# Optimization experiments

Measured on AMD Instinct MI355X. Metric: run time of the kernel, lower is better.

Reference implementation:

```python
import jax, jax.numpy as jnp
import numpy as np

B, T, D, H, L = 256, 128, 512, 512, 3  # batch, T, input_size, hidden_size, lstm layers (D == H so W_ih stacks)


def setup_inputs() -> dict:
    key = jax.random.key(0)
    ks = jax.random.split(key, 7)
    s = 0.05
    return {
        "input_data": jax.random.normal(ks[0], (B, T - 1, D), jnp.float32),
        "W_ih": jax.random.normal(ks[1], (L, 4 * H, D), jnp.float32) * s,
        "W_hh": jax.random.normal(ks[2], (L, 4 * H, H), jnp.float32) * s,
        "b_ih": jax.random.normal(ks[3], (L, 4 * H), jnp.float32) * s,
        "b_hh": jax.random.normal(ks[4], (L, 4 * H), jnp.float32) * s,
        "attn_w": jax.random.normal(ks[5], (2 * H + T - 1, 1), jnp.float32) * s,
        "attn_b": jax.random.normal(ks[6], (1,), jnp.float32) * s,
    }


def _lstm_step(x, h, c, W_ih, W_hh, b_ih, b_hh):
    # single time step of a 3-layer LSTM, PyTorch gate order (i, f, g, o)
    hs, cs = [], []
    inp = x
    for l in range(L):
        gates = inp @ W_ih[l].T + b_ih[l] + h[l] @ W_hh[l].T + b_hh[l]  # [B, 4H]
        i, f, g, o = jnp.split(gates, 4, axis=-1)
        i = jax.nn.sigmoid(i)
        f = jax.nn.sigmoid(f)
        o = jax.nn.sigmoid(o)
        g = jnp.tanh(g)
        c_new = f * c[l] + i * g
        h_new = o * jnp.tanh(c_new)
        hs.append(h_new)
        cs.append(c_new)
        inp = h_new
    return jnp.stack(hs), jnp.stack(cs)


def reference(input_data, W_ih, W_hh, b_ih, b_hh, attn_w, attn_b):
    x_perm = input_data.transpose(0, 2, 1)  # [B, D, T-1], constant across steps
    h0 = jnp.zeros((L, B, H), input_data.dtype)
    c0 = jnp.zeros_like(h0)
    xs = input_data.transpose(1, 0, 2)  # [T-1, B, D]

    def step(carry, x_t):
        h, c = carry
        # input attention uses layer-0 hidden/cell states, as in the original
        hb = jnp.broadcast_to(h[0][:, None, :], (B, D, H))
        cb = jnp.broadcast_to(c[0][:, None, :], (B, D, H))
        feat = jnp.concatenate([hb, cb, x_perm], axis=2)  # [B, D, 2H+T-1]
        logits = (feat @ attn_w)[..., 0] + attn_b[0]      # [B, D]
        attn = jax.nn.softmax(logits, axis=1)
        weighted = attn * x_t                              # [B, D]
        h, c = _lstm_step(weighted, h, c, W_ih, W_hh, b_ih, b_hh)
        return (h, c), (weighted, h[-1])

    _, (input_weighted, input_encoded) = jax.lax.scan(step, (h0, c0), xs)
    # [T-1, B, .] -> [B, T-1, .]
    return input_weighted.transpose(1, 0, 2), input_encoded.transpose(1, 0, 2)
```

## Files before the change

kernel.cpp:

```cpp
#include <hip/hip_runtime.h>
#include <math.h>

#define BATCH 256
#define TT    127
#define DD    512
#define HH    512
#define GG    2048
#define NWG   256
#define NTHR  256
#define OUT0_ELEMS ((size_t)BATCH * TT * DD)

typedef __attribute__((ext_vector_type(8))) short  short8;
typedef __attribute__((ext_vector_type(4))) float  floatx4;

__device__ __forceinline__ float bf2f(unsigned short u) {
    unsigned int x = ((unsigned int)u) << 16;
    return __builtin_bit_cast(float, x);
}
__device__ __forceinline__ unsigned short f2bf(float f) {
    unsigned int x = __builtin_bit_cast(unsigned int, f);
    unsigned int lsb = (x >> 16) & 1u;
    x += 0x7fffu + lsb;
    return (unsigned short)(x >> 16);
}

__device__ __forceinline__ int detect_is_f32(const unsigned short* p) {
    int cnt = 0;
    for (int i = 0; i < 64; ++i) {
        int e = (p[2 * i] >> 7) & 0xFF;
        cnt += (e >= 112 && e <= 133) ? 1 : 0;
    }
    return cnt < 32;
}

__device__ __forceinline__ short8 load_a8(const void* base, size_t off, int f32m) {
    if (!f32m) return *(const short8*)((const unsigned short*)base + off);
    const float* fp = (const float*)base + off;
    short8 r;
#pragma unroll
    for (int j = 0; j < 8; ++j) r[j] = (short)f2bf(fp[j]);
    return r;
}

__device__ __forceinline__ short8 load_h8(const unsigned short* p) {
    union { unsigned long long u[2]; short8 v; } t;
    t.u[0] = __hip_atomic_load((const unsigned long long*)p,
                               __ATOMIC_RELAXED, __HIP_MEMORY_SCOPE_AGENT);
    t.u[1] = __hip_atomic_load((const unsigned long long*)p + 1,
                               __ATOMIC_RELAXED, __HIP_MEMORY_SCOPE_AGENT);
    return t.v;
}

__global__ __launch_bounds__(256) void prep_kernel(
    const void* __restrict__ W_ih, const void* __restrict__ W_hh,
    const void* __restrict__ b_ih, const void* __restrict__ b_hh,
    const unsigned short* __restrict__ x_u,
    unsigned short* __restrict__ wih_bf, unsigned short* __restrict__ whh_bf,
    float* __restrict__ bsum, int* __restrict__ flag_ws)
{
    __shared__ int sflag;
    if (threadIdx.x == 0) sflag = detect_is_f32(x_u);
    __syncthreads();
    const int f32m = sflag;
    const int gid = blockIdx.x * 256 + threadIdx.x;
    const int gsz = gridDim.x * 256;
    if (gid == 0) *flag_ws = f32m;

    for (int i = gid; i < 3 * GG; i += gsz) {
        float bi = f32m ? ((const float*)b_ih)[i] : bf2f(((const unsigned short*)b_ih)[i]);
        float bh = f32m ? ((const float*)b_hh)[i] : bf2f(((const unsigned short*)b_hh)[i]);
        bsum[i] = bi + bh;
    }
    if (f32m) {
        const float* wi = (const float*)W_ih;
        const float* wh = (const float*)W_hh;
        const int n = 3 * GG * DD;
        for (int i = gid; i < n; i += gsz) {
            wih_bf[i] = f2bf(wi[i]);
            whh_bf[i] = f2bf(wh[i]);
        }
    }
}

__global__ __launch_bounds__(512) void attn_kernel(
    const void* __restrict__ xv,
    const void* __restrict__ attn_wv,
    void* __restrict__ outv,
    const int* __restrict__ flag_ws)
{
    __shared__ float red[512];
    __shared__ float wx[TT];
    __shared__ int sflag;
    const int b = blockIdx.x;
    const int d = threadIdx.x;
    if (d == 0) sflag = *flag_ws;
    __syncthreads();
    const int f32m = sflag;

    if (d < TT)
        wx[d] = f32m ? ((const float*)attn_wv)[2 * HH + d]
                     : bf2f(((const unsigned short*)attn_wv)[2 * HH + d]);
    __syncthreads();

    const size_t xb = (size_t)b * TT * DD;
    float s = 0.f;
    for (int t = 0; t < TT; ++t) {
        size_t ix = xb + (size_t)t * DD + d;
        float xval = f32m ? ((const float*)xv)[ix] : bf2f(((const unsigned short*)xv)[ix]);
        s += xval * wx[t];
    }

    red[d] = s; __syncthreads();
    for (int off = 256; off > 0; off >>= 1) {
        if (d < off) red[d] = fmaxf(red[d], red[d + off]);
        __syncthreads();
    }
    const float m = red[0]; __syncthreads();
    const float e = expf(s - m);
    red[d] = e; __syncthreads();
    for (int off = 256; off > 0; off >>= 1) {
        if (d < off) red[d] += red[d + off];
        __syncthreads();
    }
    const float a = e / red[0];

    for (int t = 0; t < TT; ++t) {
        size_t ix = xb + (size_t)t * DD + d;
        float xval = f32m ? ((const float*)xv)[ix] : bf2f(((const unsigned short*)xv)[ix]);
        float v = a * xval;
        if (f32m) ((float*)outv)[ix] = v;
        else      ((unsigned short*)outv)[ix] = f2bf(v);
    }
}

__global__ __launch_bounds__(256) void lstm_kernel(
    void* __restrict__ outv,
    const unsigned short* __restrict__ W_ih_o,
    const unsigned short* __restrict__ W_hh_o,
    const unsigned short* __restrict__ wih_bf,
    const unsigned short* __restrict__ whh_bf,
    const float* __restrict__ bsum,
    unsigned short* __restrict__ h_ws,
    unsigned* __restrict__ bar,
    const int* __restrict__ flag_ws)
{
    __shared__ float g_lds[16 * 16 * 33];
    __shared__ int sflag;
    __shared__ int s_dead;

    const int tid = threadIdx.x;
    if (tid == 0) { sflag = *flag_ws; s_dead = 0; }
    __syncthreads();
    const int f32m = sflag;

    const unsigned short* WiB = f32m ? wih_bf : W_ih_o;
    const unsigned short* WhB = f32m ? whh_bf : W_hh_o;

    const int lane   = tid & 63;
    const int wv     = tid >> 6;
    const int m_lane = lane & 15;
    const int kq     = lane >> 4;

    const int blk = blockIdx.x;
    const int xcd = blk & 7;
    const int loc = blk >> 3;
    const int hi  = xcd * 4 + (loc & 3);
    const int bi  = loc >> 2;
    const int hid0 = hi * 16;
    const int b0   = bi * 32;

    const int ep_bl = tid >> 3;
    const int ep_hp = tid & 7;

    float c_reg[3][2];
#pragma unroll
    for (int l = 0; l < 3; ++l) { c_reg[l][0] = 0.f; c_reg[l][1] = 0.f; }

    unsigned* arrv = bar + (size_t)bi * 128;
    unsigned* gen  = bar + (size_t)bi * 128 + 64;

    for (int k = 0; k < TT + 2; ++k) {
        for (int l = 0; l < 3; ++l) {
            const int t = k - l;
            if (t < 0 || t >= TT) continue;

            const unsigned short* hsrc = (l == 0) ? (const unsigned short*)0
                : (h_ws + ((size_t)(l - 1) * 2 + (t & 1)) * BATCH * HH);
            const unsigned short* hprev =
                h_ws + ((size_t)l * 2 + ((t - 1) & 1)) * BATCH * HH;
            const unsigned short* Wi = WiB + (size_t)l * GG * DD;
            const unsigned short* Wh = WhB + (size_t)l * GG * DD;

            floatx4 acc[2][4];
#pragma unroll
            for (int mt = 0; mt < 2; ++mt)
#pragma unroll
                for (int g = 0; g < 4; ++g) {
                    floatx4 z = {0.f, 0.f, 0.f, 0.f};
                    acc[mt][g] = z;
                }

#pragma unroll
            for (int kk = 0; kk < 4; ++kk) {
                const int k0 = (wv * 4 + kk) * 32 + kq * 8;
                short8 a0, a1;
                if (l == 0) {
                    a0 = load_a8(outv, ((size_t)(b0 + m_lane) * TT + t) * DD + k0, f32m);
                    a1 = load_a8(outv, ((size_t)(b0 + 16 + m_lane) * TT + t) * DD + k0, f32m);
                } else {
                    a0 = load_h8(hsrc + (size_t)(b0 + m_lane) * HH + k0);
                    a1 = load_h8(hsrc + (size_t)(b0 + 16 + m_lane) * HH + k0);
                }
#pragma unroll
                for (int g = 0; g < 4; ++g) {
                    short8 bfr = *(const short8*)(Wi + (size_t)(g * HH + hid0 + m_lane) * DD + k0);
                    acc[0][g] = __builtin_amdgcn_mfma_f32_16x16x32_bf16(a0, bfr, acc[0][g], 0, 0, 0);
                    acc[1][g] = __builtin_amdgcn_mfma_f32_16x16x32_bf16(a1, bfr, acc[1][g], 0, 0, 0);
                }
                short8 h0f = load_h8(hprev + (size_t)(b0 + m_lane) * HH + k0);
                short8 h1f = load_h8(hprev + (size_t)(b0 + 16 + m_lane) * HH + k0);
#pragma unroll
                for (int g = 0; g < 4; ++g) {
                    short8 bfr = *(const short8*)(Wh + (size_t)(g * HH + hid0 + m_lane) * DD + k0);
                    acc[0][g] = __builtin_amdgcn_mfma_f32_16x16x32_bf16(h0f, bfr, acc[0][g], 0, 0, 0);
                    acc[1][g] = __builtin_amdgcn_mfma_f32_16x16x32_bf16(h1f, bfr, acc[1][g], 0, 0, 0);
                }
            }

            __syncthreads();
#pragma unroll
            for (int mt = 0; mt < 2; ++mt)
#pragma unroll
                for (int g = 0; g < 4; ++g)
#pragma unroll
                    for (int r = 0; r < 4; ++r)
                        g_lds[((wv * 4 + g) * 16 + m_lane) * 33 + mt * 16 + kq * 4 + r]
                            = acc[mt][g][r];
            __syncthreads();

            {
                float hout[2];
#pragma unroll
                for (int dlt = 0; dlt < 2; ++dlt) {
                    const int hid = 2 * ep_hp + dlt;
                    float gv[4];
#pragma unroll
                    for (int g = 0; g < 4; ++g) {
                        float sum = 0.f;
#pragma unroll
                        for (int q = 0; q < 4; ++q)
                            sum += g_lds[((q * 4 + g) * 16 + hid) * 33 + ep_bl];
                        sum += bsum[l * GG + g * HH + hid0 + hid];
                        gv[g] = sum;
                    }
                    const float ig = 1.f / (1.f + expf(-gv[0]));
                    const float fg = 1.f / (1.f + expf(-gv[1]));
                    const float gg = tanhf(gv[2]);
                    const float og = 1.f / (1.f + expf(-gv[3]));
                    const float cnew = fg * c_reg[l][dlt] + ig * gg;
                    c_reg[l][dlt] = cnew;
                    hout[dlt] = og * tanhf(cnew);
                }
                const int bgl  = b0 + ep_bl;
                const int hidg = hid0 + 2 * ep_hp;
                const unsigned hpk = (unsigned)f2bf(hout[0])
                                   | ((unsigned)f2bf(hout[1]) << 16);
                __hip_atomic_store(
                    (unsigned*)(h_ws + (((size_t)l * 2 + (t & 1)) * BATCH + bgl) * HH + hidg),
                    hpk, __ATOMIC_RELAXED, __HIP_MEMORY_SCOPE_AGENT);
                if (l == 2) {
                    const size_t ox = OUT0_ELEMS + ((size_t)bgl * TT + t) * HH + hidg;
                    if (f32m) {
                        ((float*)outv)[ox]     = hout[0];
                        ((float*)outv)[ox + 1] = hout[1];
                    } else {
                        *(unsigned*)((unsigned short*)outv + ox) = hpk;
                    }
                }
            }
        }

        if (k < TT + 1) {
            __syncthreads();
            if (tid == 0) {
                if (!s_dead) {
                    asm volatile("s_waitcnt vmcnt(0)" ::: "memory");
                    unsigned arrived = __hip_atomic_fetch_add(arrv, 1u,
                                            __ATOMIC_RELAXED, __HIP_MEMORY_SCOPE_AGENT);
                    if (arrived == (unsigned)(k * 32 + 31)) {
                        __hip_atomic_fetch_add(gen, 1u,
                                           __ATOMIC_RELAXED, __HIP_MEMORY_SCOPE_AGENT);
                    } else {
                        int spins = 0;
                        while (__hip_atomic_load(gen, __ATOMIC_RELAXED,
                                                 __HIP_MEMORY_SCOPE_AGENT)
                               <= (unsigned)k) {
                            __builtin_amdgcn_s_sleep(2);
                            if (++spins > 8000000) { s_dead = 1; break; }
                        }
                    }
                }
            }
            __syncthreads();
        }
    }
}

#define WIH_OFF  ((size_t)0)
#define WIH_SZ   ((size_t)3 * GG * DD * 2)
#define WHH_OFF  (WIH_OFF + WIH_SZ)
#define WHH_SZ   WIH_SZ
#define BSUM_OFF (WHH_OFF + WHH_SZ)
#define BSUM_SZ  ((size_t)3 * GG * 4)
#define H_OFF    (BSUM_OFF + BSUM_SZ)
#define H_SZ     ((size_t)3 * 2 * BATCH * HH * 2)
#define BAR_OFF  (H_OFF + H_SZ)
#define BAR_SZ   ((size_t)4096)
#define FLAG_OFF (BAR_OFF + BAR_SZ)
#define WS_NEED  (FLAG_OFF + 256)

extern "C" void kernel_launch(void* const* d_in, const int* in_sizes, int n_in,
                              void* d_out, int out_size, void* d_ws, size_t ws_size,
                              hipStream_t stream) {
    (void)in_sizes; (void)n_in; (void)out_size;

    const void* x      = d_in[0];
    const void* W_ih   = d_in[1];
    const void* W_hh   = d_in[2];
    const void* b_ih   = d_in[3];
    const void* b_hh   = d_in[4];
    const void* attn_w = d_in[5];

    char* ws = (char*)d_ws;
    unsigned short* wih_bf = (unsigned short*)(ws + WIH_OFF);
    unsigned short* whh_bf = (unsigned short*)(ws + WHH_OFF);
    float*          bsum   = (float*)(ws + BSUM_OFF);
    unsigned short* h_ws   = (unsigned short*)(ws + H_OFF);
    unsigned*       bar    = (unsigned*)(ws + BAR_OFF);
    int*            flagp  = (int*)(ws + FLAG_OFF);

    if (ws_size < WS_NEED) return;

    hipMemsetAsync(ws + H_OFF, 0, H_SZ + BAR_SZ + 256, stream);

    prep_kernel<<<dim3(1024), dim3(256), 0, stream>>>(
        W_ih, W_hh, b_ih, b_hh, (const unsigned short*)x,
        wih_bf, whh_bf, bsum, flagp);

    attn_kernel<<<dim3(BATCH), dim3(512), 0, stream>>>(x, attn_w, d_out, flagp);

    lstm_kernel<<<dim3(NWG), dim3(NTHR), 0, stream>>>(
        d_out, (const unsigned short*)W_ih, (const unsigned short*)W_hh,
        wih_bf, whh_bf, bsum, h_ws, bar, flagp);
}
```

Baseline: 4.747 ms.

## Prefetch all layer hidden states per wavefront step with coherent dwordx4 loads

At the start of each wavefront step, all recurrent hidden-state fragments needed by the three layers are loaded up front with single 128-bit global loads that bypass the cache (sc0 sc1). This replaces paired 64-bit relaxed atomic loads issued inside each layer's loop. The aim is to overlap the cross-workgroup hidden-state fetch latency and halve the load instruction count. In exchange it uses many more registers, so launch bounds are set to one block per SM. It also adds a full vmcnt(0) wait and a scheduling barrier, and depends on the inline asm giving correct coherence.

```diff
diff --git a/kernel.cpp b/kernel.cpp
--- a/kernel.cpp
+++ b/kernel.cpp
@@ -12,6 +12,7 @@
 
 typedef __attribute__((ext_vector_type(8))) short  short8;
 typedef __attribute__((ext_vector_type(4))) float  floatx4;
+typedef __attribute__((ext_vector_type(4))) unsigned int uintx4;
 
 __device__ __forceinline__ float bf2f(unsigned short u) {
     unsigned int x = ((unsigned int)u) << 16;
@@ -42,13 +43,11 @@
     return r;
 }
 
-__device__ __forceinline__ short8 load_h8(const unsigned short* p) {
-    union { unsigned long long u[2]; short8 v; } t;
-    t.u[0] = __hip_atomic_load((const unsigned long long*)p,
-                               __ATOMIC_RELAXED, __HIP_MEMORY_SCOPE_AGENT);
-    t.u[1] = __hip_atomic_load((const unsigned long long*)p + 1,
-                               __ATOMIC_RELAXED, __HIP_MEMORY_SCOPE_AGENT);
-    return t.v;
+__device__ __forceinline__ short8 load_h16(const unsigned short* p) {
+    uintx4 r;
+    asm volatile("global_load_dwordx4 %0, %1, off sc0 sc1"
+                 : "=v"(r) : "v"(p));
+    return __builtin_bit_cast(short8, r);
 }
 
 __global__ __launch_bounds__(256) void prep_kernel(
@@ -133,7 +132,7 @@
     }
 }
 
-__global__ __launch_bounds__(256) void lstm_kernel(
+__global__ __launch_bounds__(256, 1) void lstm_kernel(
     void* __restrict__ outv,
     const unsigned short* __restrict__ W_ih_o,
     const unsigned short* __restrict__ W_hh_o,
@@ -180,14 +179,28 @@
     unsigned* gen  = bar + (size_t)bi * 128 + 64;
 
     for (int k = 0; k < TT + 2; ++k) {
+        short8 pfb[3][4][2];
+#pragma unroll
+        for (int j = 0; j < 3; ++j) {
+            const int kj = k - j;
+            if (kj < 0 || kj > TT) continue;
+            const unsigned short* hb =
+                h_ws + ((size_t)j * 2 + ((kj - 1) & 1)) * BATCH * HH;
+#pragma unroll
+            for (int kk = 0; kk < 4; ++kk) {
+                const int k0 = (wv * 4 + kk) * 32 + kq * 8;
+                pfb[j][kk][0] = load_h16(hb + (size_t)(b0 + m_lane) * HH + k0);
+                pfb[j][kk][1] = load_h16(hb + (size_t)(b0 + 16 + m_lane) * HH + k0);
+            }
+        }
+        asm volatile("s_waitcnt vmcnt(0)" ::: "memory");
+        __builtin_amdgcn_sched_barrier(0);
+
+#pragma unroll
         for (int l = 0; l < 3; ++l) {
             const int t = k - l;
             if (t < 0 || t >= TT) continue;
 
-            const unsigned short* hsrc = (l == 0) ? (const unsigned short*)0
-                : (h_ws + ((size_t)(l - 1) * 2 + (t & 1)) * BATCH * HH);
-            const unsigned short* hprev =
-                h_ws + ((size_t)l * 2 + ((t - 1) & 1)) * BATCH * HH;
             const unsigned short* Wi = WiB + (size_t)l * GG * DD;
             const unsigned short* Wh = WhB + (size_t)l * GG * DD;
 
@@ -208,8 +221,8 @@
                     a0 = load_a8(outv, ((size_t)(b0 + m_lane) * TT + t) * DD + k0, f32m);
                     a1 = load_a8(outv, ((size_t)(b0 + 16 + m_lane) * TT + t) * DD + k0, f32m);
                 } else {
-                    a0 = load_h8(hsrc + (size_t)(b0 + m_lane) * HH + k0);
-                    a1 = load_h8(hsrc + (size_t)(b0 + 16 + m_lane) * HH + k0);
+                    a0 = pfb[l - 1][kk][0];
+                    a1 = pfb[l - 1][kk][1];
                 }
 #pragma unroll
                 for (int g = 0; g < 4; ++g) {
@@ -217,8 +230,8 @@
                     acc[0][g] = __builtin_amdgcn_mfma_f32_16x16x32_bf16(a0, bfr, acc[0][g], 0, 0, 0);
                     acc[1][g] = __builtin_amdgcn_mfma_f32_16x16x32_bf16(a1, bfr, acc[1][g], 0, 0, 0);
                 }
-                short8 h0f = load_h8(hprev + (size_t)(b0 + m_lane) * HH + k0);
-                short8 h1f = load_h8(hprev + (size_t)(b0 + 16 + m_lane) * HH + k0);
+                short8 h0f = pfb[l][kk][0];
+                short8 h1f = pfb[l][kk][1];
 #pragma unroll
                 for (int g = 0; g < 4; ++g) {
                     short8 bfr = *(const short8*)(Wh + (size_t)(g * HH + hid0 + m_lane) * DD + k0);
```

After: 4.271 ms. 10.0% less time.
